# Optimization experiments

Measured on AMD Instinct MI355X. Metric: run time of the kernel, lower is better.

Reference implementation:

```python
import jax, jax.numpy as jnp
import numpy as np

B, S, DIM = 2, 4096, 768
G = DIM // 3          # gate_dim = 256
H, DK = 4, G // 4     # heads=4, d_k=64
SCALE = 1.0 / np.sqrt(DK)


def setup_inputs() -> dict:
    key = jax.random.key(0)
    ks = jax.random.split(key, 9)
    r = lambda k, shp, s: (jax.random.normal(k, shp, dtype=jnp.float32) * s)
    w_s = 1.0 / np.sqrt(G)
    return {
        "x": r(ks[0], (B, S, DIM), 1.0),
        "wq": r(ks[1], (G, G), w_s), "bq": r(ks[2], (G,), 0.01),
        "wk": r(ks[3], (G, G), w_s), "bk": r(ks[4], (G,), 0.01),
        "wv": r(ks[5], (G, G), w_s), "bv": r(ks[6], (G,), 0.01),
        "wo": r(ks[7], (G, G), w_s), "bo": r(ks[8], (G,), 0.01),
    }


def reference(x, wq, bq, wk, bk, wv, bv, wo, bo):
    # chunk(3, dim=-1): q/k/v slices of width G
    xq, xk, xv = x[..., :G], x[..., G:2 * G], x[..., 2 * G:3 * G]
    # linear projections then split into heads: [b, s, h, d]
    q = (xq @ wq.T + bq).reshape(B, S, H, DK)
    k = (xk @ wk.T + bk).reshape(B, S, H, DK)
    v = (xv @ wv.T + bv).reshape(B, S, H, DK)
    scores = jnp.einsum('bihd,bjhd->bijh', q, k) * SCALE  # [b, i, j, h]
    # NOTE: original applies Softmax(dim=1) -> over the QUERY axis i
    attn = jax.nn.softmax(scores, axis=1)
    out = jnp.einsum('bijh,bjhd->bihd', attn, v).reshape(B, S, G)
    return out @ wo.T + bo
```

## Files before the change

### kernel.cpp

```cpp
#include <hip/hip_runtime.h>

#define SEQ   4096
#define HH    4
#define SCALE 0.125f
#define SC2   0.18033688011112042f
#define C16   -23.083120654223414f

typedef __bf16 bf16x8 __attribute__((ext_vector_type(8)));
typedef __bf16 bf16x4 __attribute__((ext_vector_type(4)));
typedef float  f32x4  __attribute__((ext_vector_type(4)));

constexpr size_t OFF_W16  = 0;
constexpr size_t OFF_A    = 131072;
constexpr size_t OFF_AO   = 294912;
constexpr size_t OFF_X16  = 9732096;
constexpr size_t OFF_Q16  = 12877824;
constexpr size_t K16OFF   = 2097152;
constexpr size_t V16OFF   = 4194304;
constexpr size_t OFF_PZ   = 16023552;

__device__ __forceinline__ f32x4 mf(bf16x8 a, bf16x8 b, f32x4 c) {
    return __builtin_amdgcn_mfma_f32_16x16x32_bf16(a, b, c, 0, 0, 0);
}

__device__ __forceinline__ void gload16(const __bf16* g, __bf16* l) {
    __builtin_amdgcn_global_load_lds(
        (const __attribute__((address_space(1))) unsigned int*)g,
        (__attribute__((address_space(3))) unsigned int*)l, 16, 0, 0);
}

__device__ __forceinline__ float ex2(float x) {
    return __builtin_amdgcn_exp2f(x);
}

__global__ void k_prep(const float* __restrict__ x,
                       const float* __restrict__ wq, const float* __restrict__ wk,
                       const float* __restrict__ wv, const float* __restrict__ wo,
                       float* __restrict__ ws) {
    int bx = blockIdx.x, t = threadIdx.x;
    if (bx < 6144) {
        size_t i4 = ((size_t)bx * 256 + t) * 4;
        float4 v = *(const float4*)(x + i4);
        bf16x4 o = {(__bf16)v.x, (__bf16)v.y, (__bf16)v.z, (__bf16)v.w};
        *(bf16x4*)((__bf16*)(ws + OFF_X16) + i4) = o;
    } else if (bx < 6400) {
        int q = bx - 6144;
        int y = q >> 6;
        const float* src = (y == 0) ? wq : (y == 1) ? wk : (y == 2) ? wv : wo;
        float sc = (y == 0) ? SC2 : 1.0f;
        size_t i4 = ((size_t)(q & 63) * 256 + t) * 4;
        float4 v = *(const float4*)(src + i4);
        bf16x4 o = {(__bf16)(v.x * sc), (__bf16)(v.y * sc),
                    (__bf16)(v.z * sc), (__bf16)(v.w * sc)};
        *(bf16x4*)((__bf16*)(ws + OFF_W16) + (size_t)y * 65536 + i4) = o;
    } else {
        size_t i4 = ((size_t)(bx - 6400) * 256 + t) * 4;
        *(float4*)(ws + OFF_AO + i4) = make_float4(0.f, 0.f, 0.f, 0.f);
    }
}

__global__ __launch_bounds__(256) void k_qkv_mfma(const float* __restrict__ bq,
                                                  const float* __restrict__ bk,
                                                  const float* __restrict__ bv,
                                                  float* __restrict__ ws) {
    int t = threadIdx.x, lane = t & 63, w = t >> 6;
    int yw = blockIdx.y;
    int ntb = blockIdx.z * 8;
    int row0 = blockIdx.x * 64 + w * 16;
    int mrow = lane & 15, quad = lane >> 4;
    const __bf16* X16 = (const __bf16*)(ws + OFF_X16);
    const __bf16* W16 = (const __bf16*)(ws + OFF_W16) + (size_t)yw * 65536;
    const float* bias = (yw == 0) ? bq : (yw == 1) ? bk : bv;
    __bf16* Qb = (__bf16*)(ws + OFF_Q16);
    f32x4 acc[8];
#pragma unroll
    for (int n = 0; n < 8; n++) acc[n] = {0.f, 0.f, 0.f, 0.f};
    const __bf16* ap = X16 + (size_t)(row0 + mrow) * 768 + yw * 256 + quad * 8;
    const __bf16* bp = W16 + (size_t)ntb * 4096 + (size_t)mrow * 256 + quad * 8;
    for (int kc = 0; kc < 256; kc += 32) {
        bf16x8 a = *(const bf16x8*)(ap + kc);
#pragma unroll
        for (int nt = 0; nt < 8; nt++) {
            bf16x8 b = *(const bf16x8*)(bp + (size_t)nt * 4096 + kc);
            acc[nt] = mf(a, b, acc[nt]);
        }
    }
#pragma unroll
    for (int nt = 0; nt < 8; nt++) {
        int n = (ntb + nt) * 16 + mrow;
        float bb = bias[n];
        if (yw == 0) bb *= SC2;
        int h = n >> 6, d = n & 63;
#pragma unroll
        for (int r = 0; r < 4; r++) {
            int sg = row0 + quad * 4 + r;
            int b_ = sg >> 12, s = sg & 4095;
            int bh = b_ * HH + h;
            float val = acc[nt][r] + bb;
            if (yw == 0) {
                int tile = s >> 4, m = s & 15, frag = d >> 5, q2 = (d >> 3) & 3, e = d & 7;
                size_t idx = (((size_t)bh * 256 + tile) * 2 + frag) * 512 +
                             (size_t)(q2 * 16 + m) * 8 + e;
                Qb[idx] = (__bf16)val;
            } else if (yw == 1) {
                int jc = s >> 5, jj = s & 31;
                int tl = (jj >> 2) & 1, m = ((jj >> 3) << 2) | (jj & 3);
                int frag = d >> 5, q2 = (d >> 3) & 3, e = d & 7;
                size_t idx = (((size_t)bh * 128 + jc) * 4 + tl * 2 + frag) * 512 +
                             (size_t)(q2 * 16 + m) * 8 + e;
                Qb[K16OFF + idx] = (__bf16)val;
            } else {
                int jc = s >> 5, qk = (s >> 3) & 3, e = s & 7;
                int nd = d >> 4, nl = d & 15;
                size_t idx = (((size_t)bh * 128 + jc) * 4 + nd) * 512 +
                             (size_t)(qk * 16 + nl) * 8 + e;
                Qb[V16OFF + idx] = (__bf16)val;
            }
        }
    }
}

__global__ __launch_bounds__(256) void k_colstats(float* __restrict__ ws) {
    __shared__ __bf16 qbuf[2][4096];
    int t = threadIdx.x, lane = t & 63, w = t >> 6;
    int jb = blockIdx.x, iy = blockIdx.y, bh = blockIdx.z;
    int jc = jb * 4 + w;
    const __bf16* Qp = (const __bf16*)(ws + OFF_Q16);
    const __bf16* Kp = Qp + K16OFF;
    const __bf16* kb = Kp + ((size_t)(bh * 128 + jc) * 4) * 512 + lane * 8;
    bf16x8 bk00 = *(const bf16x8*)(kb);
    bf16x8 bk01 = *(const bf16x8*)(kb + 512);
    bf16x8 bk10 = *(const bf16x8*)(kb + 1024);
    bf16x8 bk11 = *(const bf16x8*)(kb + 1536);
    const __bf16* q0 = Qp + ((size_t)(bh * 256 + iy * 32) * 2) * 512 +
                       w * 1024 + lane * 8;
    gload16(q0, qbuf[0] + w * 1024);
    gload16(q0 + 512, qbuf[0] + w * 1024 + 512);
    __syncthreads();
    const f32x4 cin = {C16, C16, C16, C16};
    float z0 = 0.f, z1 = 0.f;
    for (int ic = 0; ic < 8; ic++) {
        const __bf16* cur = qbuf[ic & 1];
        if (ic < 7) {
            const __bf16* qn = Qp + ((size_t)(bh * 256 + iy * 32 + (ic + 1) * 4) * 2) * 512 +
                               w * 1024 + lane * 8;
            gload16(qn, qbuf[(ic + 1) & 1] + w * 1024);
            gload16(qn + 512, qbuf[(ic + 1) & 1] + w * 1024 + 512);
        }
#pragma unroll
        for (int it = 0; it < 4; it++) {
            bf16x8 a0 = *(const bf16x8*)(cur + it * 1024 + lane * 8);
            bf16x8 a1 = *(const bf16x8*)(cur + it * 1024 + 512 + lane * 8);
            f32x4 c0 = mf(a0, bk00, cin);
            c0 = mf(a1, bk01, c0);
            f32x4 c1 = mf(a0, bk10, cin);
            c1 = mf(a1, bk11, c1);
#pragma unroll
            for (int r = 0; r < 4; r++) {
                z0 += ex2(c0[r]);
                z1 += ex2(c1[r]);
            }
        }
        __syncthreads();
    }
    z0 += __shfl_xor(z0, 16, 64);
    z0 += __shfl_xor(z0, 32, 64);
    z1 += __shfl_xor(z1, 16, 64);
    z1 += __shfl_xor(z1, 32, 64);
    if (lane < 16) {
        size_t o = OFF_PZ + (size_t)iy * 32768 + (size_t)bh * SEQ +
                   jc * 32 + ((lane >> 2) << 3) + (lane & 3);
        ws[o] = z0;
        ws[o + 4] = z1;
    }
}

__global__ void k_afin(float* __restrict__ ws) {
    int idx = blockIdx.x * 256 + threadIdx.x;
    const float* pz = ws + OFF_PZ;
    float Z = 0.f;
#pragma unroll
    for (int y = 0; y < 8; y++) Z += pz[(size_t)y * 32768 + idx];
    ws[OFF_A + idx] = C16 - __log2f(Z);
}

__global__ __launch_bounds__(256) void k_attnpv(float* __restrict__ ws) {
    __shared__ __align__(16) char pool[17408];
    __bf16* ldsK = (__bf16*)pool;
    __bf16* ldsV = (__bf16*)(pool + 8192);
    int t = threadIdx.x, lane = t & 63, w = t >> 6;
    int jy = blockIdx.y, bh = blockIdx.z;
    int itp = blockIdx.x * 4 + w;
    int it0 = itp * 2;
    int mrow = lane & 15, quad = lane >> 4;
    const __bf16* Qp = (const __bf16*)(ws + OFF_Q16);
    const __bf16* Kp = Qp + K16OFF;
    const __bf16* Vp = Qp + V16OFF;
    const float* Ag = ws + OFF_A + (size_t)bh * SEQ + jy * 1024 + quad * 8;

    const __bf16* qb = Qp + ((size_t)(bh * 256 + it0) * 2) * 512 + lane * 8;
    bf16x8 aq00 = *(const bf16x8*)(qb);
    bf16x8 aq01 = *(const bf16x8*)(qb + 512);
    bf16x8 aq10 = *(const bf16x8*)(qb + 1024);
    bf16x8 aq11 = *(const bf16x8*)(qb + 1536);

    f32x4 oT0[4], oT1[4];
#pragma unroll
    for (int nd = 0; nd < 4; nd++) {
        oT0[nd] = {0.f, 0.f, 0.f, 0.f};
        oT1[nd] = {0.f, 0.f, 0.f, 0.f};
    }
    int c0g = jy * 32;
    const __bf16* kg = Kp + ((size_t)(bh * 128 + c0g) * 4) * 512 + w * 512 + lane * 8;
    const __bf16* vg = Vp + ((size_t)(bh * 128 + c0g) * 4) * 512 + w * 512 + lane * 8;
    gload16(kg, ldsK + w * 512);
    gload16(vg, ldsV + w * 512);
    kg += 2048; vg += 2048;
    f32x4 aL = *(const f32x4*)(Ag);
    f32x4 aH = *(const f32x4*)(Ag + 4);
    __syncthreads();

    for (int jt = 0; jt < 32; jt++) {
        const __bf16* curK = ldsK + (jt & 1) * 2048;
        const __bf16* curV = ldsV + (jt & 1) * 2048;
        f32x4 aLn = aL, aHn = aH;
        if (jt < 31) {
            gload16(kg, ldsK + ((jt + 1) & 1) * 2048 + w * 512);
            gload16(vg, ldsV + ((jt + 1) & 1) * 2048 + w * 512);
            kg += 2048; vg += 2048;
            aLn = *(const f32x4*)(Ag + (jt + 1) * 32);
            aHn = *(const f32x4*)(Ag + (jt + 1) * 32 + 4);
        }
        bf16x8 ck0 = *(const bf16x8*)(curK + lane * 8);
        bf16x8 ck1 = *(const bf16x8*)(curK + 512 + lane * 8);
        bf16x8 ck2 = *(const bf16x8*)(curK + 1024 + lane * 8);
        bf16x8 ck3 = *(const bf16x8*)(curK + 1536 + lane * 8);
        f32x4 c00 = mf(ck0, aq00, aL); c00 = mf(ck1, aq01, c00);
        f32x4 c01 = mf(ck2, aq00, aH); c01 = mf(ck3, aq01, c01);
        f32x4 c10 = mf(ck0, aq10, aL); c10 = mf(ck1, aq11, c10);
        f32x4 c11 = mf(ck2, aq10, aH); c11 = mf(ck3, aq11, c11);
        bf16x8 pb0, pb1;
#pragma unroll
        for (int r = 0; r < 4; r++) {
            pb0[r]     = (__bf16)ex2(c00[r]);
            pb0[4 + r] = (__bf16)ex2(c01[r]);
            pb1[r]     = (__bf16)ex2(c10[r]);
            pb1[4 + r] = (__bf16)ex2(c11[r]);
        }
#pragma unroll
        for (int nd = 0; nd < 4; nd++) {
            bf16x8 bv = *(const bf16x8*)(curV + nd * 512 + lane * 8);
            oT0[nd] = mf(bv, pb0, oT0[nd]);
            oT1[nd] = mf(bv, pb1, oT1[nd]);
        }
        aL = aLn; aH = aHn;
        __syncthreads();
    }

    float* sO = (float*)pool + (size_t)w * 1040;
    int b = bh >> 2, h = bh & 3;
    float* AO = ws + OFF_AO;
    int i0 = it0 * 16;
#pragma unroll
    for (int nd = 0; nd < 4; nd++)
#pragma unroll
        for (int r = 0; r < 4; r++)
            sO[mrow * 65 + nd * 16 + quad * 4 + r] = oT0[nd][r];
#pragma unroll
    for (int c = 0; c < 16; c++)
        atomicAdd(&AO[((size_t)(b * SEQ + i0 + c)) * 256 + h * 64 + lane],
                  sO[c * 65 + lane]);
#pragma unroll
    for (int nd = 0; nd < 4; nd++)
#pragma unroll
        for (int r = 0; r < 4; r++)
            sO[mrow * 65 + nd * 16 + quad * 4 + r] = oT1[nd][r];
#pragma unroll
    for (int c = 0; c < 16; c++)
        atomicAdd(&AO[((size_t)(b * SEQ + i0 + 16 + c)) * 256 + h * 64 + lane],
                  sO[c * 65 + lane]);
}

__global__ __launch_bounds__(256) void k_outproj_mfma(const float* __restrict__ bo,
                                                      float* __restrict__ ws,
                                                      float* __restrict__ out) {
    int t = threadIdx.x, lane = t & 63, w = t >> 6;
    int row0 = blockIdx.x * 64 + w * 16;
    int ntb = blockIdx.y * 4;
    int mrow = lane & 15, quad = lane >> 4;
    const float* AO = ws + OFF_AO;
    const __bf16* W16 = (const __bf16*)(ws + OFF_W16) + (size_t)3 * 65536;
    f32x4 acc[4];
#pragma unroll
    for (int n = 0; n < 4; n++) acc[n] = {0.f, 0.f, 0.f, 0.f};
    const float* ap = AO + (size_t)(row0 + mrow) * 256 + quad * 8;
    const __bf16* bp = W16 + (size_t)ntb * 4096 + (size_t)mrow * 256 + quad * 8;
    for (int kc = 0; kc < 256; kc += 32) {
        float4 u = *(const float4*)(ap + kc);
        float4 v = *(const float4*)(ap + kc + 4);
        bf16x8 a = {(__bf16)u.x, (__bf16)u.y, (__bf16)u.z, (__bf16)u.w,
                    (__bf16)v.x, (__bf16)v.y, (__bf16)v.z, (__bf16)v.w};
#pragma unroll
        for (int nt = 0; nt < 4; nt++) {
            bf16x8 b = *(const bf16x8*)(bp + (size_t)nt * 4096 + kc);
            acc[nt] = mf(a, b, acc[nt]);
        }
    }
#pragma unroll
    for (int nt = 0; nt < 4; nt++) {
        int n = (ntb + nt) * 16 + mrow;
        float bb = bo[n];
#pragma unroll
        for (int r = 0; r < 4; r++) {
            int sg = row0 + quad * 4 + r;
            out[(size_t)sg * 256 + n] = acc[nt][r] + bb;
        }
    }
}

extern "C" void kernel_launch(void* const* d_in, const int* in_sizes, int n_in,
                              void* d_out, int out_size, void* d_ws, size_t ws_size,
                              hipStream_t stream) {
    const float* x  = (const float*)d_in[0];
    const float* wq = (const float*)d_in[1];
    const float* bq = (const float*)d_in[2];
    const float* wk = (const float*)d_in[3];
    const float* bk = (const float*)d_in[4];
    const float* wv = (const float*)d_in[5];
    const float* bv = (const float*)d_in[6];
    const float* wo = (const float*)d_in[7];
    const float* bo = (const float*)d_in[8];
    float* ws = (float*)d_ws;
    float* out = (float*)d_out;

    k_prep<<<8448, 256, 0, stream>>>(x, wq, wk, wv, wo, ws);
    k_qkv_mfma<<<dim3(128, 3, 2), 256, 0, stream>>>(bq, bk, bv, ws);
    k_colstats<<<dim3(32, 8, 8), 256, 0, stream>>>(ws);
    k_afin<<<128, 256, 0, stream>>>(ws);
    k_attnpv<<<dim3(32, 4, 8), 256, 0, stream>>>(ws);
    k_outproj_mfma<<<dim3(128, 4), 256, 0, stream>>>(bo, ws, out);
}
```

Baseline: 213.5 us.

## Retile column-stats and attention kernels, load V fragments directly from global

k_colstats now gives each wave two key chunks (four accumulators) over half as many query tiles. It launches 16x16 blocks and writes 16 partial-sum slices, which k_afin now reduces. k_attnpv splits the key axis into 8 slices instead of 4, doubling the grid. It also drops the LDS double buffer for V and reads V fragments straight from global memory into registers each iteration. The aim is more parallelism and more K register reuse, at the cost of twice as many atomicAdd partial outputs, a larger PZ workspace, and V load latency that is no longer hidden behind the LDS prefetch.

After: 227.0 us. 6.3% more time.

```diff
diff --git a/kernel.cpp b/kernel.cpp
--- a/kernel.cpp
+++ b/kernel.cpp
@@ -124,25 +124,29 @@
     __shared__ __bf16 qbuf[2][4096];
     int t = threadIdx.x, lane = t & 63, w = t >> 6;
     int jb = blockIdx.x, iy = blockIdx.y, bh = blockIdx.z;
-    int jc = jb * 4 + w;
+    int jc0 = jb * 8 + w * 2;
     const __bf16* Qp = (const __bf16*)(ws + OFF_Q16);
     const __bf16* Kp = Qp + K16OFF;
-    const __bf16* kb = Kp + ((size_t)(bh * 128 + jc) * 4) * 512 + lane * 8;
-    bf16x8 bk00 = *(const bf16x8*)(kb);
-    bf16x8 bk01 = *(const bf16x8*)(kb + 512);
-    bf16x8 bk10 = *(const bf16x8*)(kb + 1024);
-    bf16x8 bk11 = *(const bf16x8*)(kb + 1536);
-    const __bf16* q0 = Qp + ((size_t)(bh * 256 + iy * 32) * 2) * 512 +
+    const __bf16* kb = Kp + ((size_t)(bh * 128 + jc0) * 4) * 512 + lane * 8;
+    bf16x8 kA0 = *(const bf16x8*)(kb);
+    bf16x8 kA1 = *(const bf16x8*)(kb + 512);
+    bf16x8 kB0 = *(const bf16x8*)(kb + 1024);
+    bf16x8 kB1 = *(const bf16x8*)(kb + 1536);
+    bf16x8 kC0 = *(const bf16x8*)(kb + 2048);
+    bf16x8 kC1 = *(const bf16x8*)(kb + 2560);
+    bf16x8 kD0 = *(const bf16x8*)(kb + 3072);
+    bf16x8 kD1 = *(const bf16x8*)(kb + 3584);
+    const __bf16* q0 = Qp + ((size_t)(bh * 256 + iy * 16) * 2) * 512 +
                        w * 1024 + lane * 8;
     gload16(q0, qbuf[0] + w * 1024);
     gload16(q0 + 512, qbuf[0] + w * 1024 + 512);
     __syncthreads();
     const f32x4 cin = {C16, C16, C16, C16};
-    float z0 = 0.f, z1 = 0.f;
-    for (int ic = 0; ic < 8; ic++) {
+    float z0 = 0.f, z1 = 0.f, z2 = 0.f, z3 = 0.f;
+    for (int ic = 0; ic < 4; ic++) {
         const __bf16* cur = qbuf[ic & 1];
-        if (ic < 7) {
-            const __bf16* qn = Qp + ((size_t)(bh * 256 + iy * 32 + (ic + 1) * 4) * 2) * 512 +
+        if (ic < 3) {
+            const __bf16* qn = Qp + ((size_t)(bh * 256 + iy * 16 + (ic + 1) * 4) * 2) * 512 +
                                w * 1024 + lane * 8;
             gload16(qn, qbuf[(ic + 1) & 1] + w * 1024);
             gload16(qn + 512, qbuf[(ic + 1) & 1] + w * 1024 + 512);
@@ -151,14 +155,16 @@
         for (int it = 0; it < 4; it++) {
             bf16x8 a0 = *(const bf16x8*)(cur + it * 1024 + lane * 8);
             bf16x8 a1 = *(const bf16x8*)(cur + it * 1024 + 512 + lane * 8);
-            f32x4 c0 = mf(a0, bk00, cin);
-            c0 = mf(a1, bk01, c0);
-            f32x4 c1 = mf(a0, bk10, cin);
-            c1 = mf(a1, bk11, c1);
+            f32x4 cA = mf(a0, kA0, cin); cA = mf(a1, kA1, cA);
+            f32x4 cB = mf(a0, kB0, cin); cB = mf(a1, kB1, cB);
+            f32x4 cC = mf(a0, kC0, cin); cC = mf(a1, kC1, cC);
+            f32x4 cD = mf(a0, kD0, cin); cD = mf(a1, kD1, cD);
 #pragma unroll
             for (int r = 0; r < 4; r++) {
-                z0 += ex2(c0[r]);
-                z1 += ex2(c1[r]);
+                z0 += ex2(cA[r]);
+                z1 += ex2(cB[r]);
+                z2 += ex2(cC[r]);
+                z3 += ex2(cD[r]);
             }
         }
         __syncthreads();
@@ -167,11 +173,17 @@
     z0 += __shfl_xor(z0, 32, 64);
     z1 += __shfl_xor(z1, 16, 64);
     z1 += __shfl_xor(z1, 32, 64);
+    z2 += __shfl_xor(z2, 16, 64);
+    z2 += __shfl_xor(z2, 32, 64);
+    z3 += __shfl_xor(z3, 16, 64);
+    z3 += __shfl_xor(z3, 32, 64);
     if (lane < 16) {
         size_t o = OFF_PZ + (size_t)iy * 32768 + (size_t)bh * SEQ +
-                   jc * 32 + ((lane >> 2) << 3) + (lane & 3);
+                   jc0 * 32 + ((lane >> 2) << 3) + (lane & 3);
         ws[o] = z0;
         ws[o + 4] = z1;
+        ws[o + 32] = z2;
+        ws[o + 36] = z3;
     }
 }
 
@@ -180,14 +192,13 @@
     const float* pz = ws + OFF_PZ;
     float Z = 0.f;
 #pragma unroll
-    for (int y = 0; y < 8; y++) Z += pz[(size_t)y * 32768 + idx];
+    for (int y = 0; y < 16; y++) Z += pz[(size_t)y * 32768 + idx];
     ws[OFF_A + idx] = C16 - __log2f(Z);
 }
 
 __global__ __launch_bounds__(256) void k_attnpv(float* __restrict__ ws) {
     __shared__ __align__(16) char pool[17408];
     __bf16* ldsK = (__bf16*)pool;
-    __bf16* ldsV = (__bf16*)(pool + 8192);
     int t = threadIdx.x, lane = t & 63, w = t >> 6;
     int jy = blockIdx.y, bh = blockIdx.z;
     int itp = blockIdx.x * 4 + w;
@@ -196,7 +207,7 @@
     const __bf16* Qp = (const __bf16*)(ws + OFF_Q16);
     const __bf16* Kp = Qp + K16OFF;
     const __bf16* Vp = Qp + V16OFF;
-    const float* Ag = ws + OFF_A + (size_t)bh * SEQ + jy * 1024 + quad * 8;
+    const float* Ag = ws + OFF_A + (size_t)bh * SEQ + jy * 512 + quad * 8;
 
     const __bf16* qb = Qp + ((size_t)(bh * 256 + it0) * 2) * 512 + lane * 8;
     bf16x8 aq00 = *(const bf16x8*)(qb);
@@ -210,24 +221,26 @@
         oT0[nd] = {0.f, 0.f, 0.f, 0.f};
         oT1[nd] = {0.f, 0.f, 0.f, 0.f};
     }
-    int c0g = jy * 32;
+    int c0g = jy * 16;
     const __bf16* kg = Kp + ((size_t)(bh * 128 + c0g) * 4) * 512 + w * 512 + lane * 8;
-    const __bf16* vg = Vp + ((size_t)(bh * 128 + c0g) * 4) * 512 + w * 512 + lane * 8;
     gload16(kg, ldsK + w * 512);
-    gload16(vg, ldsV + w * 512);
-    kg += 2048; vg += 2048;
+    kg += 2048;
+    const __bf16* vgb = Vp + ((size_t)(bh * 128 + c0g) * 4) * 512 + lane * 8;
     f32x4 aL = *(const f32x4*)(Ag);
     f32x4 aH = *(const f32x4*)(Ag + 4);
     __syncthreads();
 
-    for (int jt = 0; jt < 32; jt++) {
+    for (int jt = 0; jt < 16; jt++) {
         const __bf16* curK = ldsK + (jt & 1) * 2048;
-        const __bf16* curV = ldsV + (jt & 1) * 2048;
+        bf16x8 bv0 = *(const bf16x8*)(vgb);
+        bf16x8 bv1 = *(const bf16x8*)(vgb + 512);
+        bf16x8 bv2 = *(const bf16x8*)(vgb + 1024);
+        bf16x8 bv3 = *(const bf16x8*)(vgb + 1536);
+        vgb += 2048;
         f32x4 aLn = aL, aHn = aH;
-        if (jt < 31) {
+        if (jt < 15) {
             gload16(kg, ldsK + ((jt + 1) & 1) * 2048 + w * 512);
-            gload16(vg, ldsV + ((jt + 1) & 1) * 2048 + w * 512);
-            kg += 2048; vg += 2048;
+            kg += 2048;
             aLn = *(const f32x4*)(Ag + (jt + 1) * 32);
             aHn = *(const f32x4*)(Ag + (jt + 1) * 32 + 4);
         }
@@ -247,12 +260,14 @@
             pb1[r]     = (__bf16)ex2(c10[r]);
             pb1[4 + r] = (__bf16)ex2(c11[r]);
         }
-#pragma unroll
-        for (int nd = 0; nd < 4; nd++) {
-            bf16x8 bv = *(const bf16x8*)(curV + nd * 512 + lane * 8);
-            oT0[nd] = mf(bv, pb0, oT0[nd]);
-            oT1[nd] = mf(bv, pb1, oT1[nd]);
-        }
+        oT0[0] = mf(bv0, pb0, oT0[0]);
+        oT1[0] = mf(bv0, pb1, oT1[0]);
+        oT0[1] = mf(bv1, pb0, oT0[1]);
+        oT1[1] = mf(bv1, pb1, oT1[1]);
+        oT0[2] = mf(bv2, pb0, oT0[2]);
+        oT1[2] = mf(bv2, pb1, oT1[2]);
+        oT0[3] = mf(bv3, pb0, oT0[3]);
+        oT1[3] = mf(bv3, pb1, oT1[3]);
         aL = aLn; aH = aHn;
         __syncthreads();
     }
@@ -335,8 +350,8 @@
 
     k_prep<<<8448, 256, 0, stream>>>(x, wq, wk, wv, wo, ws);
     k_qkv_mfma<<<dim3(128, 3, 2), 256, 0, stream>>>(bq, bk, bv, ws);
-    k_colstats<<<dim3(32, 8, 8), 256, 0, stream>>>(ws);
+    k_colstats<<<dim3(16, 16, 8), 256, 0, stream>>>(ws);
     k_afin<<<128, 256, 0, stream>>>(ws);
-    k_attnpv<<<dim3(32, 4, 8), 256, 0, stream>>>(ws);
+    k_attnpv<<<dim3(32, 8, 8), 256, 0, stream>>>(ws);
     k_outproj_mfma<<<dim3(128, 4), 256, 0, stream>>>(bo, ws, out);
 }
```
